# Kernel tuning notes

Measured on AMD Instinct MI355X. Metric: run time of the kernel, lower is better.

The kernel has to match this reference:

```python
import jax, jax.numpy as jnp
import numpy as np

N_NODES = 50000
N_EDGES = 400000
D_NODE = 256
D_EDGE = 64
LN_EPS = 1e-6  # flax LayerNorm default


def _layer_norm(x, scale, bias):
    mu = jnp.mean(x, axis=-1, keepdims=True)
    var = jnp.mean(jnp.square(x - mu), axis=-1, keepdims=True)
    return (x - mu) * jax.lax.rsqrt(var + LN_EPS) * scale + bias


def _glorot(key, shape):
    fan_in, fan_out = shape
    std = jnp.sqrt(2.0 / (fan_in + fan_out))
    return std * jax.random.normal(key, shape, dtype=jnp.float32)


def setup_inputs() -> dict:
    key = jax.random.key(0)
    ks = jax.random.split(key, 10)
    inp = {
        "nodes": jax.random.normal(ks[0], (N_NODES, D_NODE), dtype=jnp.float32),
        "edges": jax.random.normal(ks[1], (N_EDGES, D_EDGE), dtype=jnp.float32),
        "senders": jax.random.randint(ks[2], (N_EDGES,), 0, N_NODES, dtype=jnp.int32),
        "receivers": jax.random.randint(ks[3], (N_EDGES,), 0, N_NODES, dtype=jnp.int32),
        # message projection (no bias)
        "W_message": _glorot(ks[4], (D_NODE + D_EDGE, D_NODE)),
        # NodeMLP (ReluMLP_skip) with n_features_list_nodes = [256, 256, 256]
        "mlp_W0": _glorot(ks[5], (D_NODE, D_NODE)), "mlp_b0": jnp.zeros((D_NODE,), jnp.float32),
        "mlp_W1": _glorot(ks[6], (D_NODE, D_NODE)), "mlp_b1": jnp.zeros((D_NODE,), jnp.float32),
        "mlp_W2": _glorot(ks[7], (D_NODE, D_NODE)), "mlp_b2": jnp.zeros((D_NODE,), jnp.float32),
        # LayerNorm params
        "ln_aggr_scale": jnp.ones((D_NODE,), jnp.float32), "ln_aggr_bias": jnp.zeros((D_NODE,), jnp.float32),
        "ln_out_scale": jnp.ones((D_NODE,), jnp.float32), "ln_out_bias": jnp.zeros((D_NODE,), jnp.float32),
    }
    return inp


def _relu_mlp_skip(x, Ws, bs):
    # Dense layers; ReLU on all but the last; residual add whenever widths match.
    n = len(Ws)
    for i, (W, b) in enumerate(zip(Ws, bs)):
        y = x @ W + b
        if i < n - 1:
            y = jax.nn.relu(y)
        x = x + y if y.shape[-1] == x.shape[-1] else y
    return x


def reference(nodes, edges, senders, receivers, W_message,
              mlp_W0, mlp_b0, mlp_W1, mlp_b1, mlp_W2, mlp_b2,
              ln_aggr_scale, ln_aggr_bias, ln_out_scale, ln_out_bias):
    total_nodes = nodes.shape[0]
    sender_features = nodes[senders]                      # [E, d] gather
    msg_in = jnp.concatenate([sender_features, edges], axis=-1)  # [E, d+d_e]
    messages = msg_in @ W_message                          # [E, d]
    agg = jax.ops.segment_sum(messages, receivers, num_segments=total_nodes)  # [N, d]
    h = _layer_norm(jax.nn.relu(agg) + nodes, ln_aggr_scale, ln_aggr_bias)
    nodes_out = _relu_mlp_skip(h, [mlp_W0, mlp_W1, mlp_W2], [mlp_b0, mlp_b1, mlp_b2])
    nodes_new = _layer_norm(nodes + nodes_out, ln_out_scale, ln_out_bias)
    return nodes_new
```

## Files before the change

kernel.cpp:

```cpp
#include <hip/hip_runtime.h>

#define NN 50000
#define NE 400000

typedef unsigned short u16;
typedef unsigned int   u32;
typedef __bf16 bf16x4 __attribute__((ext_vector_type(4)));
typedef __bf16 bf16x8 __attribute__((ext_vector_type(8)));
typedef float  f32x4  __attribute__((ext_vector_type(4)));

union ABFrag { bf16x8 v; bf16x4 h[2]; };
union BFrag  { uint4 u; bf16x8 v; };

__device__ __forceinline__ u16 f2bfu(float f) {
  u32 u = __builtin_bit_cast(u32, f);
  return (u16)((u + 0x7FFFu + ((u >> 16) & 1u)) >> 16);
}
__device__ __forceinline__ float bf2f(u16 u) {
  return __builtin_bit_cast(float, (u32)u << 16);
}

__device__ __forceinline__ void pack_one(const float* __restrict__ W,
                                         u16* __restrict__ P, int idx) {
  int k = idx >> 8, n = idx & 255;
  int t = k >> 5, kp = k & 31;
  int g = (kp & 15) >> 2;
  int j = (kp & 3) | ((kp >> 4) << 2);
  P[(((t << 8) + n) << 5) + (g << 3) + j] = f2bfu(W[idx]);
}

#define NB_CVT  12500
#define NB_PACK 1088
#define NB_HIST 1563

__global__ __launch_bounds__(256) void k_prep(
    const float* __restrict__ nodes, u16* __restrict__ nodes_bf,
    const float* __restrict__ Wm, const float* __restrict__ W0,
    const float* __restrict__ W1, const float* __restrict__ W2,
    u16* __restrict__ Pm, u16* __restrict__ P0,
    u16* __restrict__ P1, u16* __restrict__ P2,
    const int* __restrict__ recv, int* __restrict__ cnt)
{
  int b = blockIdx.x, t = threadIdx.x;
  if (b < NB_CVT) {
    int i = b * 256 + t;
    float4 f = ((const float4*)nodes)[i];
    ushort4 o;
    o.x = f2bfu(f.x); o.y = f2bfu(f.y); o.z = f2bfu(f.z); o.w = f2bfu(f.w);
    ((ushort4*)nodes_bf)[i] = o;
  } else if (b < NB_CVT + NB_PACK) {
    int idx = (b - NB_CVT) * 256 + t;
    const int S0 = 320 * 256, S1 = S0 + 65536, S2 = S1 + 65536;
    if (idx < S0)      pack_one(Wm, Pm, idx);
    else if (idx < S1) pack_one(W0, P0, idx - S0);
    else if (idx < S2) pack_one(W1, P1, idx - S1);
    else               pack_one(W2, P2, idx - S2);
  } else {
    int i = (b - NB_CVT - NB_PACK) * 256 + t;
    if (i < NE) atomicAdd(&cnt[recv[i]], 1);
  }
}

__global__ __launch_bounds__(256) void k_scan1(const int* __restrict__ cnt,
                                               int* __restrict__ loc,
                                               int* __restrict__ bsum) {
  __shared__ int sm[256];
  int t = threadIdx.x, i = blockIdx.x * 256 + t;
  int v = (i < NN) ? cnt[i] : 0;
  sm[t] = v;
  __syncthreads();
  #pragma unroll
  for (int d = 1; d < 256; d <<= 1) {
    int x = sm[t];
    int y = (t >= d) ? sm[t - d] : 0;
    __syncthreads();
    sm[t] = x + y;
    __syncthreads();
  }
  if (i < NN) loc[i] = sm[t] - v;
  if (t == 255) bsum[blockIdx.x] = sm[255];
}

__global__ __launch_bounds__(256) void k_scan2(int* __restrict__ bsum,
                                               int* __restrict__ bpre, int nb) {
  __shared__ int sm[256];
  int t = threadIdx.x;
  int v = (t < nb) ? bsum[t] : 0;
  sm[t] = v;
  __syncthreads();
  #pragma unroll
  for (int d = 1; d < 256; d <<= 1) {
    int x = sm[t];
    int y = (t >= d) ? sm[t - d] : 0;
    __syncthreads();
    sm[t] = x + y;
    __syncthreads();
  }
  if (t < nb) bpre[t] = sm[t] - v;
}

__global__ __launch_bounds__(256) void k_scan3(const int* __restrict__ loc,
                                               const int* __restrict__ bpre,
                                               int* __restrict__ offs,
                                               int* __restrict__ cursor) {
  int i = blockIdx.x * 256 + threadIdx.x;
  if (i < NN) {
    int o = loc[i] + bpre[blockIdx.x];
    offs[i] = o;
    cursor[i] = o;
  }
  if (i == NN - 1) offs[NN] = NE;
}

__global__ __launch_bounds__(256) void k_scatter(
    const int* __restrict__ snd, const int* __restrict__ recv,
    int* __restrict__ cursor, int* __restrict__ s_snd, int* __restrict__ s_eid) {
  int e = blockIdx.x * 256 + threadIdx.x;
  if (e < NE) {
    int p = atomicAdd(&cursor[recv[e]], 1);
    s_snd[p] = snd[e];
    s_eid[p] = e;
  }
}

__global__ __launch_bounds__(256) void k_aggr(
    const u16* __restrict__ nodes_bf, const float* __restrict__ edges,
    const int* __restrict__ offs, const int* __restrict__ s_snd,
    const int* __restrict__ s_eid, u16* __restrict__ X)
{
  const int wid = blockIdx.x * 4 + (threadIdx.x >> 6);
  const int lane = threadIdx.x & 63;
  const int n0 = wid * 4;
  const int o0 = offs[n0], b1 = offs[n0 + 1], b2 = offs[n0 + 2],
            b3 = offs[n0 + 3], o4 = offs[n0 + 4];

  float a0 = 0.f, a1 = 0.f, a2 = 0.f, a3 = 0.f, a4 = 0.f;
  int cur = 0;

#define AGLD(J, NV, EV) do { int _j = (J); if (_j < o4) { \
    int _s = s_snd[_j], _e = s_eid[_j]; \
    NV = *(const ushort4*)(nodes_bf + (size_t)_s * 256 + (lane << 2)); \
    EV = edges[(size_t)_e * 64 + lane]; } } while (0)

#define AGFLUSH(NODE) do { \
    ushort4 _o; _o.x = f2bfu(a0); _o.y = f2bfu(a1); _o.z = f2bfu(a2); _o.w = f2bfu(a3); \
    u16* _xr = X + (size_t)(NODE) * 320; \
    *(ushort4*)(_xr + (lane << 2)) = _o; \
    _xr[256 + lane] = f2bfu(a4); \
    a0 = 0.f; a1 = 0.f; a2 = 0.f; a3 = 0.f; a4 = 0.f; } while (0)

#define AGCONS(J, NV, EV) do { int _j = (J); if (_j < o4) { \
    if (cur == 0 && _j == b1) { AGFLUSH(n0);     cur = 1; } \
    if (cur == 1 && _j == b2) { AGFLUSH(n0 + 1); cur = 2; } \
    if (cur == 2 && _j == b3) { AGFLUSH(n0 + 2); cur = 3; } \
    a0 += bf2f(NV.x); a1 += bf2f(NV.y); a2 += bf2f(NV.z); a3 += bf2f(NV.w); \
    a4 += EV; } } while (0)

  ushort4 v0 = {0,0,0,0}, v1 = {0,0,0,0}, v2 = {0,0,0,0}, v3 = {0,0,0,0};
  float e0 = 0.f, e1 = 0.f, e2 = 0.f, e3 = 0.f;
  AGLD(o0 + 0, v0, e0); AGLD(o0 + 1, v1, e1);
  AGLD(o0 + 2, v2, e2); AGLD(o0 + 3, v3, e3);

  for (int jb = o0; jb < o4; jb += 4) {
    ushort4 w0 = {0,0,0,0}, w1 = {0,0,0,0}, w2 = {0,0,0,0}, w3 = {0,0,0,0};
    float f0 = 0.f, f1 = 0.f, f2 = 0.f, f3 = 0.f;
    AGLD(jb + 4, w0, f0); AGLD(jb + 5, w1, f1);
    AGLD(jb + 6, w2, f2); AGLD(jb + 7, w3, f3);
    AGCONS(jb + 0, v0, e0); AGCONS(jb + 1, v1, e1);
    AGCONS(jb + 2, v2, e2); AGCONS(jb + 3, v3, e3);
    v0 = w0; v1 = w1; v2 = w2; v3 = w3;
    e0 = f0; e1 = f1; e2 = f2; e3 = f3;
  }
  for (int k = cur; k < 4; ++k) AGFLUSH(n0 + k);
#undef AGLD
#undef AGFLUSH
#undef AGCONS
}


#define AT_ADDR(r, c) (atb + ((((r) * 640) + ((c) * 2)) ^ (((r) & 7) << 4)))

#define WRBT(c, v) do { int _c = (c); \
  int _i = (((_c >> 10) << 13) + ((_c & 3) << 11) + (((_c & 1023) >> 2) << 3)) ^ ((_c & 3) << 4); \
  *(uint4*)&Bt[_i] = (v); } while (0)

#define MFMA_STEP(t) \
  _Pragma("unroll") \
  for (int kk = 0; kk < 2; ++kk) { \
    ABFrag a; \
    const int kc = (((t) * 2 + kk) << 5) + (g << 2); \
    const int m = wr16 + l16; \
    a.h[0] = *(const bf16x4*)AT_ADDR(m, kc); \
    a.h[1] = *(const bf16x4*)AT_ADDR(m, kc + 16); \
    _Pragma("unroll") \
    for (int q = 0; q < 4; ++q) { \
      BFrag b; \
      b.u = *(const uint4*)&Bt[((kk << 13) + (g << 11) + ((wcn + (q << 4) + l16) << 3)) ^ (g << 4)]; \
      acc[q] = __builtin_amdgcn_mfma_f32_16x16x32_bf16(a.v, b.v, acc[q], 0, 0, 0); \
    } \
  }

#define RUN_LAYER(wp, T) do { \
  const u16* pb = (wp) + ((size_t)tid << 3); \
  uint4 p0 = *(const uint4*)(pb); \
  uint4 p1 = *(const uint4*)(pb + 8192); \
  _Pragma("unroll 1") \
  for (int t = 0; t < (T); ++t) { \
    __syncthreads(); \
    WRBT(tid, p0); WRBT(tid + 1024, p1); \
    __syncthreads(); \
    if (t + 1 < (T)) {                      \
      const u16* nb = pb + ((size_t)(t + 1) << 14); \
      p0 = *(const uint4*)nb; p1 = *(const uint4*)(nb + 8192); \
    } \
    MFMA_STEP(t) \
  } \
} while (0)

#define LN_STATS() do { \
  _Pragma("unroll") \
  for (int r = 0; r < 4; ++r) { \
    float s  = acc[0][r] + acc[1][r] + acc[2][r] + acc[3][r]; \
    float s2 = acc[0][r]*acc[0][r] + acc[1][r]*acc[1][r] + acc[2][r]*acc[2][r] + acc[3][r]*acc[3][r]; \
    s  += __shfl_xor(s, 1);  s  += __shfl_xor(s, 2);  s  += __shfl_xor(s, 4);  s  += __shfl_xor(s, 8); \
    s2 += __shfl_xor(s2, 1); s2 += __shfl_xor(s2, 2); s2 += __shfl_xor(s2, 4); s2 += __shfl_xor(s2, 8); \
    if (l16 == 0) { int m = wr16 + g4 + r; red[m][wc2] = s; red[m][wc2 + 1] = s2; } \
  } \
  __syncthreads(); \
  if (tid < 64) { \
    float s  = red[tid][0] + red[tid][2] + red[tid][4] + red[tid][6]; \
    float s2 = red[tid][1] + red[tid][3] + red[tid][5] + red[tid][7]; \
    float mu  = s * (1.f / 256.f); \
    float var = s2 * (1.f / 256.f) - mu * mu; \
    murs[tid][0] = mu; murs[tid][1] = rsqrtf(var + 1e-6f); \
  } \
  __syncthreads(); \
} while (0)

__global__ __launch_bounds__(1024)
void k_fused(
    const u16* __restrict__ X, const float* __restrict__ nodes,
    const u16* __restrict__ wm, const u16* __restrict__ w0,
    const u16* __restrict__ w1, const u16* __restrict__ w2,
    const float* __restrict__ b0, const float* __restrict__ b1,
    const float* __restrict__ b2,
    const float* __restrict__ lnAs, const float* __restrict__ lnAb,
    const float* __restrict__ lnOs, const float* __restrict__ lnOb,
    float* __restrict__ out)
{
  __shared__ u16 At[64 * 320];
  __shared__ u16 Bt[16384];
  __shared__ float red[64][8];
  __shared__ float murs[64][2];

  const int tid = threadIdx.x;
  const int lane = tid & 63;
  const int w16 = tid >> 6;
  const int wr16 = (w16 >> 2) << 4;
  const int wcn = (w16 & 3) << 6;
  const int wc2 = (w16 & 3) << 1;
  const int l16 = lane & 15, g = lane >> 4, g4 = g << 2;
  const int r0 = blockIdx.x * 64;

  char* const atb = (char*)At;

  #pragma unroll
  for (int it = 0; it < 3; ++it) {
    int c = tid + it * 1024;
    if (c < 2560) {
      int r = c / 40, seg = c - r * 40;
      int row = r0 + r;
      uint4 v = {0u, 0u, 0u, 0u};
      if (row < NN) v = *(const uint4*)(X + (size_t)row * 320 + seg * 8);
      *(uint4*)(atb + ((r * 640 + seg * 16) ^ ((r & 7) << 4))) = v;
    }
  }

  f32x4 acc[4];
  const f32x4 z = {0.f, 0.f, 0.f, 0.f};
  #pragma unroll
  for (int q = 0; q < 4; ++q) acc[q] = z;

  RUN_LAYER(wm, 5);

  #pragma unroll
  for (int q = 0; q < 4; ++q) {
    int n = wcn + (q << 4) + l16;
    #pragma unroll
    for (int r = 0; r < 4; ++r) {
      int row = r0 + wr16 + g4 + r;
      float nv = (row < NN) ? nodes[(size_t)row * 256 + n] : 0.f;
      acc[q][r] = fmaxf(acc[q][r], 0.f) + nv;
    }
  }
  LN_STATS();
  #pragma unroll
  for (int q = 0; q < 4; ++q) {
    int n = wcn + (q << 4) + l16;
    float scl = lnAs[n], bia = lnAb[n];
    #pragma unroll
    for (int r = 0; r < 4; ++r) {
      int m = wr16 + g4 + r;
      float h = (acc[q][r] - murs[m][0]) * murs[m][1] * scl + bia;
      *(u16*)AT_ADDR(m, n) = f2bfu(h);
      acc[q][r] = 0.f;
    }
  }

  #pragma unroll 1
  for (int l = 0; l < 3; ++l) {
    const u16* wp = (l == 0) ? w0 : (l == 1) ? w1 : w2;
    RUN_LAYER(wp, 4);
    __syncthreads();

    if (l < 2) {
      const float* bp = (l == 0) ? b0 : b1;
      #pragma unroll
      for (int q = 0; q < 4; ++q) {
        int n = wcn + (q << 4) + l16;
        float bn = bp[n];
        #pragma unroll
        for (int r = 0; r < 4; ++r) {
          int m = wr16 + g4 + r;
          u16* p = (u16*)AT_ADDR(m, n);
          float xn = bf2f(*p) + fmaxf(acc[q][r] + bn, 0.f);
          *p = f2bfu(xn);
          acc[q][r] = 0.f;
        }
      }
    } else {
      #pragma unroll
      for (int q = 0; q < 4; ++q) {
        int n = wcn + (q << 4) + l16;
        float bn = b2[n];
        #pragma unroll
        for (int r = 0; r < 4; ++r) {
          int m = wr16 + g4 + r;
          int row = r0 + m;
          float nv = (row < NN) ? nodes[(size_t)row * 256 + n] : 0.f;
          acc[q][r] = nv + bf2f(*(const u16*)AT_ADDR(m, n)) + acc[q][r] + bn;
        }
      }
    }
  }

  LN_STATS();
  #pragma unroll
  for (int q = 0; q < 4; ++q) {
    int n = wcn + (q << 4) + l16;
    float scl = lnOs[n], bia = lnOb[n];
    #pragma unroll
    for (int r = 0; r < 4; ++r) {
      int m = wr16 + g4 + r;
      int row = r0 + m;
      if (row < NN)
        out[(size_t)row * 256 + n] =
            (acc[q][r] - murs[m][0]) * murs[m][1] * scl + bia;
    }
  }
}

extern "C" void kernel_launch(void* const* d_in, const int* in_sizes, int n_in,
                              void* d_out, int out_size, void* d_ws, size_t ws_size,
                              hipStream_t stream)
{
  const float* nodes = (const float*)d_in[0];
  const float* edges = (const float*)d_in[1];
  const int* senders = (const int*)d_in[2];
  const int* receivers = (const int*)d_in[3];
  const float* Wmsg = (const float*)d_in[4];
  const float* W0 = (const float*)d_in[5];
  const float* b0 = (const float*)d_in[6];
  const float* W1 = (const float*)d_in[7];
  const float* b1 = (const float*)d_in[8];
  const float* W2 = (const float*)d_in[9];
  const float* b2 = (const float*)d_in[10];
  const float* lnAs = (const float*)d_in[11];
  const float* lnAb = (const float*)d_in[12];
  const float* lnOs = (const float*)d_in[13];
  const float* lnOb = (const float*)d_in[14];
  float* out = (float*)d_out;
  (void)in_sizes; (void)n_in; (void)out_size; (void)ws_size;

  char* w = (char*)d_ws;
  size_t off = 0;
  auto take = [&](size_t b) { void* p = w + off; off += (b + 511) & ~(size_t)511; return p; };

  u16*   nodes_bf = (u16*)take((size_t)NN * 256 * 2);
  u16*   wmsg_p   = (u16*)take(320 * 256 * 2);
  u16*   w0_p     = (u16*)take(256 * 256 * 2);
  u16*   w1_p     = (u16*)take(256 * 256 * 2);
  u16*   w2_p     = (u16*)take(256 * 256 * 2);
  u16*   X        = (u16*)take((size_t)NN * 320 * 2);
  int*   cnt      = (int*)take((size_t)NN * 4);
  int*   loc      = (int*)take((size_t)NN * 4);
  int*   offs     = (int*)take((size_t)(NN + 1) * 4);
  int*   cursor   = (int*)take((size_t)NN * 4);
  int*   s_snd    = (int*)take((size_t)NE * 4);
  int*   s_eid    = (int*)take((size_t)NE * 4);
  int*   bsum     = (int*)take(256 * 4);
  int*   bpre     = (int*)take(256 * 4);

  const int NB = (NN + 255) / 256;

  hipMemsetAsync(cnt, 0, (size_t)NN * 4, stream);
  k_prep<<<NB_CVT + NB_PACK + NB_HIST, 256, 0, stream>>>(
      nodes, nodes_bf, Wmsg, W0, W1, W2, wmsg_p, w0_p, w1_p, w2_p,
      receivers, cnt);

  k_scan1<<<NB, 256, 0, stream>>>(cnt, loc, bsum);
  k_scan2<<<1, 256, 0, stream>>>(bsum, bpre, NB);
  k_scan3<<<NB, 256, 0, stream>>>(loc, bpre, offs, cursor);
  k_scatter<<<(NE + 255) / 256, 256, 0, stream>>>(senders, receivers, cursor, s_snd, s_eid);

  k_aggr<<<NN / 16, 256, 0, stream>>>(nodes_bf, edges, offs, s_snd, s_eid, X);

  const int MB = (NN + 63) / 64;
  k_fused<<<MB, 1024, 0, stream>>>(X, nodes, wmsg_p, w0_p, w1_p, w2_p,
                                   b0, b1, b2, lnAs, lnAb, lnOs, lnOb, out);
}
```

Baseline: 248.4 us.

## Assign one wavefront per node and batch-gather edges via shuffled index pairs

The aggregation kernel now gives each wavefront a single receiver node instead of four. Each 8-edge batch is handled by one coalesced load of (sender, edge-id) pairs, which are then broadcast with lane shuffles, so eight row gathers are in flight at once. The scatter stage writes the sender and edge index into one interleaved int2 array instead of two separate arrays. This removes the serial per-node flush logic and the per-edge scalar index loads, and raises the grid fourfold. The cost is wasted gather loads on partial batches, because tail lanes are clamped to the last edge and the loads still issue.

Measured after the change: 225.7 us. -9.1%, faster.

```diff
diff --git a/kernel.cpp b/kernel.cpp
--- a/kernel.cpp
+++ b/kernel.cpp
@@ -114,69 +114,57 @@
 
 __global__ __launch_bounds__(256) void k_scatter(
     const int* __restrict__ snd, const int* __restrict__ recv,
-    int* __restrict__ cursor, int* __restrict__ s_snd, int* __restrict__ s_eid) {
+    int* __restrict__ cursor, int2* __restrict__ s_pair) {
   int e = blockIdx.x * 256 + threadIdx.x;
   if (e < NE) {
     int p = atomicAdd(&cursor[recv[e]], 1);
-    s_snd[p] = snd[e];
-    s_eid[p] = e;
+    int2 pr; pr.x = snd[e]; pr.y = e;
+    s_pair[p] = pr;
   }
 }
 
 __global__ __launch_bounds__(256) void k_aggr(
     const u16* __restrict__ nodes_bf, const float* __restrict__ edges,
-    const int* __restrict__ offs, const int* __restrict__ s_snd,
-    const int* __restrict__ s_eid, u16* __restrict__ X)
+    const int* __restrict__ offs, const int2* __restrict__ s_pair,
+    u16* __restrict__ X)
 {
-  const int wid = blockIdx.x * 4 + (threadIdx.x >> 6);
+  const int node = blockIdx.x * 4 + (threadIdx.x >> 6);
   const int lane = threadIdx.x & 63;
-  const int n0 = wid * 4;
-  const int o0 = offs[n0], b1 = offs[n0 + 1], b2 = offs[n0 + 2],
-            b3 = offs[n0 + 3], o4 = offs[n0 + 4];
-
+  const int beg = offs[node], end = offs[node + 1];
   float a0 = 0.f, a1 = 0.f, a2 = 0.f, a3 = 0.f, a4 = 0.f;
-  int cur = 0;
-
-#define AGLD(J, NV, EV) do { int _j = (J); if (_j < o4) { \
-    int _s = s_snd[_j], _e = s_eid[_j]; \
-    NV = *(const ushort4*)(nodes_bf + (size_t)_s * 256 + (lane << 2)); \
-    EV = edges[(size_t)_e * 64 + lane]; } } while (0)
-
-#define AGFLUSH(NODE) do { \
-    ushort4 _o; _o.x = f2bfu(a0); _o.y = f2bfu(a1); _o.z = f2bfu(a2); _o.w = f2bfu(a3); \
-    u16* _xr = X + (size_t)(NODE) * 320; \
-    *(ushort4*)(_xr + (lane << 2)) = _o; \
-    _xr[256 + lane] = f2bfu(a4); \
-    a0 = 0.f; a1 = 0.f; a2 = 0.f; a3 = 0.f; a4 = 0.f; } while (0)
-
-#define AGCONS(J, NV, EV) do { int _j = (J); if (_j < o4) { \
-    if (cur == 0 && _j == b1) { AGFLUSH(n0);     cur = 1; } \
-    if (cur == 1 && _j == b2) { AGFLUSH(n0 + 1); cur = 2; } \
-    if (cur == 2 && _j == b3) { AGFLUSH(n0 + 2); cur = 3; } \
-    a0 += bf2f(NV.x); a1 += bf2f(NV.y); a2 += bf2f(NV.z); a3 += bf2f(NV.w); \
-    a4 += EV; } } while (0)
-
-  ushort4 v0 = {0,0,0,0}, v1 = {0,0,0,0}, v2 = {0,0,0,0}, v3 = {0,0,0,0};
-  float e0 = 0.f, e1 = 0.f, e2 = 0.f, e3 = 0.f;
-  AGLD(o0 + 0, v0, e0); AGLD(o0 + 1, v1, e1);
-  AGLD(o0 + 2, v2, e2); AGLD(o0 + 3, v3, e3);
-
-  for (int jb = o0; jb < o4; jb += 4) {
-    ushort4 w0 = {0,0,0,0}, w1 = {0,0,0,0}, w2 = {0,0,0,0}, w3 = {0,0,0,0};
-    float f0 = 0.f, f1 = 0.f, f2 = 0.f, f3 = 0.f;
-    AGLD(jb + 4, w0, f0); AGLD(jb + 5, w1, f1);
-    AGLD(jb + 6, w2, f2); AGLD(jb + 7, w3, f3);
-    AGCONS(jb + 0, v0, e0); AGCONS(jb + 1, v1, e1);
-    AGCONS(jb + 2, v2, e2); AGCONS(jb + 3, v3, e3);
-    v0 = w0; v1 = w1; v2 = w2; v3 = w3;
-    e0 = f0; e1 = f1; e2 = f2; e3 = f3;
-  }
-  for (int k = cur; k < 4; ++k) AGFLUSH(n0 + k);
-#undef AGLD
-#undef AGFLUSH
-#undef AGCONS
-}
-
+
+  for (int jb = beg; jb < end; jb += 8) {
+    int j = jb + (lane & 7);
+    if (j >= end) j = end - 1;
+    int2 pr = s_pair[j];
+    const int rem = end - jb;
+
+#define GATHER(K) \
+    int s##K = __shfl(pr.x, K); int e##K = __shfl(pr.y, K); \
+    ushort4 n##K = *(const ushort4*)(nodes_bf + (size_t)s##K * 256 + (lane << 2)); \
+    float v##K = edges[(size_t)e##K * 64 + lane];
+
+    GATHER(0) GATHER(1) GATHER(2) GATHER(3)
+    GATHER(4) GATHER(5) GATHER(6) GATHER(7)
+#undef GATHER
+
+#define ACCUM(K) \
+    if (rem > K) { \
+      a0 += bf2f(n##K.x); a1 += bf2f(n##K.y); \
+      a2 += bf2f(n##K.z); a3 += bf2f(n##K.w); \
+      a4 += v##K; }
+
+    ACCUM(0) ACCUM(1) ACCUM(2) ACCUM(3)
+    ACCUM(4) ACCUM(5) ACCUM(6) ACCUM(7)
+#undef ACCUM
+  }
+
+  u16* xr = X + (size_t)node * 320;
+  ushort4 o;
+  o.x = f2bfu(a0); o.y = f2bfu(a1); o.z = f2bfu(a2); o.w = f2bfu(a3);
+  *(ushort4*)(xr + (lane << 2)) = o;
+  xr[256 + lane] = f2bfu(a4);
+}
 
 #define AT_ADDR(r, c) (atb + ((((r) * 640) + ((c) * 2)) ^ (((r) & 7) << 4)))
 
@@ -209,7 +197,7 @@
     __syncthreads(); \
     WRBT(tid, p0); WRBT(tid + 1024, p1); \
     __syncthreads(); \
-    if (t + 1 < (T)) {                      \
+    if (t + 1 < (T)) { \
       const u16* nb = pb + ((size_t)(t + 1) << 14); \
       p0 = *(const uint4*)nb; p1 = *(const uint4*)(nb + 8192); \
     } \
@@ -396,8 +384,7 @@
   int*   loc      = (int*)take((size_t)NN * 4);
   int*   offs     = (int*)take((size_t)(NN + 1) * 4);
   int*   cursor   = (int*)take((size_t)NN * 4);
-  int*   s_snd    = (int*)take((size_t)NE * 4);
-  int*   s_eid    = (int*)take((size_t)NE * 4);
+  int2*  s_pair   = (int2*)take((size_t)NE * 8);
   int*   bsum     = (int*)take(256 * 4);
   int*   bpre     = (int*)take(256 * 4);
 
@@ -411,9 +398,9 @@
   k_scan1<<<NB, 256, 0, stream>>>(cnt, loc, bsum);
   k_scan2<<<1, 256, 0, stream>>>(bsum, bpre, NB);
   k_scan3<<<NB, 256, 0, stream>>>(loc, bpre, offs, cursor);
-  k_scatter<<<(NE + 255) / 256, 256, 0, stream>>>(senders, receivers, cursor, s_snd, s_eid);
-
-  k_aggr<<<NN / 16, 256, 0, stream>>>(nodes_bf, edges, offs, s_snd, s_eid, X);
+  k_scatter<<<(NE + 255) / 256, 256, 0, stream>>>(senders, receivers, cursor, s_pair);
+
+  k_aggr<<<NN / 4, 256, 0, stream>>>(nodes_bf, edges, offs, s_pair, X);
 
   const int MB = (NN + 63) / 64;
   k_fused<<<MB, 1024, 0, stream>>>(X, nodes, wmsg_p, w0_p, w1_p, w2_p,
```
